# Optimization experiments

Hardware: AMD Instinct MI355X
Metric: run time of the kernel (lower is better)

The kernel has to match this reference:

```python
import jax, jax.numpy as jnp
import numpy as np

EPS = 1e-5

def ste_sign(x):
    # forward: sign(x) in {-1,+1}; backward: straight-through with |x|<=1 clip
    xc = jnp.clip(x, -1.0, 1.0)
    s = jnp.where(x >= 0, 1.0, -1.0).astype(x.dtype)
    return xc + jax.lax.stop_gradient(s - xc)

def quant_w(w):
    # 1-bit weight: sign(w) scaled by mean |w| (XNOR-Net style)
    return ste_sign(w) * jnp.mean(jnp.abs(w))

def qconv(x, w, stride, pad):
    # quantized conv: binarize activations and weights, then dense conv
    xq = ste_sign(x)
    wq = quant_w(w)
    return jax.lax.conv_general_dilated(
        xq, wq, window_strides=(stride, stride),
        padding=[(pad, pad), (pad, pad)],
        dimension_numbers=('NCHW', 'OIHW', 'NCHW'))

def batchnorm(x, gamma, beta):
    # training-mode BN: batch statistics over (N, H, W)
    mu = jnp.mean(x, axis=(0, 2, 3), keepdims=True)
    var = jnp.var(x, axis=(0, 2, 3), keepdims=True)
    xhat = (x - mu) * jax.lax.rsqrt(var + EPS)
    return xhat * gamma[None, :, None, None] + beta[None, :, None, None]

def setup_inputs() -> dict:
    key = jax.random.key(0)
    ks = jax.random.split(key, 4)
    in_planes, planes = 128, 256
    x = jax.random.normal(ks[0], (64, in_planes, 56, 56), dtype=jnp.float32)
    w1 = jax.random.normal(ks[1], (planes, in_planes, 3, 3), dtype=jnp.float32) * 0.05
    w2 = jax.random.normal(ks[2], (planes, planes, 3, 3), dtype=jnp.float32) * 0.05
    ws = jax.random.normal(ks[3], (planes, in_planes, 1, 1), dtype=jnp.float32) * 0.05
    g1 = jnp.ones((planes,), jnp.float32); b1 = jnp.zeros((planes,), jnp.float32)
    g2 = jnp.ones((planes,), jnp.float32); b2 = jnp.zeros((planes,), jnp.float32)
    return {'x': x, 'w1': w1, 'g1': g1, 'b1': b1, 'w2': w2, 'g2': g2, 'b2': b2, 'ws': ws}

def reference(x, w1, g1, b1, w2, g2, b2, ws):
    out = batchnorm(qconv(x, w1, stride=2, pad=1), g1, b1)   # [N,256,28,28]
    out = qconv(out, w2, stride=1, pad=1)
    out = out + qconv(x, ws, stride=2, pad=0)                # quantized 1x1 shortcut
    out = batchnorm(out, g2, b2)
    return out
```

## Files before the change

kernel.cpp:

```cpp
#include <hip/hip_runtime.h>
#include <stdint.h>

#define N_    64
#define CIN   128
#define CMID  256
#define H_    56
#define W_    56
#define OH    28
#define OW    28
#define NPIX  (OH*OW)
#define MPAD  800
#define MTOT  (N_*MPAD)
#define CNT_CH (N_*NPIX)
#define PXH   58
#define PYH   30
#define EPS_  1e-5f

#define STATS_BYTES 16384
#define OFF_PXI 16384
#define OFF_PYI (OFF_PXI + 27551744)
#define OFF_W1F (OFF_PYI + 14745600)
#define OFF_W2F (OFF_W1F + 294912)
#define OFF_WSF (OFF_W2F + 589824)
#define MEMSET_BYTES OFF_W1F

typedef int v4i  __attribute__((ext_vector_type(4)));
typedef int v16i __attribute__((ext_vector_type(16)));

#define MFMA_I8 __builtin_amdgcn_mfma_i32_32x32x32_i8

typedef const __attribute__((address_space(1))) void* gas_t;
typedef __attribute__((address_space(3))) void* las_t;

__device__ __forceinline__ void gl_lds16(const void* g, void* l) {
  __builtin_amdgcn_global_load_lds((gas_t)g, (las_t)l, 16, 0, 0);
}

__global__ __launch_bounds__(256) void reduce_abs_k(const float* __restrict__ w, int n,
                                                    float* __restrict__ out) {
  float s = 0.f;
  for (int i = blockIdx.x * 256 + threadIdx.x; i < n; i += gridDim.x * 256)
    s += fabsf(w[i]);
  for (int off = 32; off; off >>= 1) s += __shfl_down(s, off);
  if ((threadIdx.x & 63) == 0) atomicAdd(out, s);
}

__global__ __launch_bounds__(256) void pack_x_k(const float* __restrict__ x,
                                                int8_t* __restrict__ px) {
  int idx = blockIdx.x * 256 + threadIdx.x;
  int n = idx / (H_ * W_), hw = idx - n * (H_ * W_);
  int ih = hw / W_, iw = hw - ih * W_;
  const float* xp = x + ((size_t)n * CIN) * (H_ * W_) + hw;
  uint32_t wd[32];
#pragma unroll
  for (int c4 = 0; c4 < 32; ++c4) {
    uint32_t wv = 0u;
#pragma unroll
    for (int j = 0; j < 4; ++j) {
      uint32_t b = (xp[(size_t)(c4 * 4 + j) * (H_ * W_)] >= 0.f) ? 0x01u : 0xFFu;
      wv |= b << (j * 8);
    }
    wd[c4] = wv;
  }
  uint4* dst = (uint4*)(px + (((size_t)n * (PXH * PXH) + (ih + 1) * PXH + (iw + 1)) * CIN));
#pragma unroll
  for (int q = 0; q < 8; ++q)
    dst[q] = make_uint4(wd[q * 4], wd[q * 4 + 1], wd[q * 4 + 2], wd[q * 4 + 3]);
}

__global__ __launch_bounds__(256) void packw1f_k(const float* __restrict__ w1,
                                                 uint32_t* __restrict__ w1f) {
  int T = blockIdx.x * 256 + threadIdx.x;
  int l = T & 63, fb = T >> 6;
  int nb = fb & 7, kc = fb >> 3;
  int o = nb * 32 + (l & 31);
  int kbase = kc * 32 + (l >> 5) * 16;
  uint32_t wd[4] = {0u, 0u, 0u, 0u};
#pragma unroll
  for (int j = 0; j < 16; ++j) {
    int k = kbase + j, t = k >> 7, c = k & 127;
    uint32_t b = (w1[((size_t)o * CIN + c) * 9 + t] >= 0.f) ? 0x01u : 0xFFu;
    wd[j >> 2] |= b << ((j & 3) * 8);
  }
  ((uint4*)w1f)[T] = make_uint4(wd[0], wd[1], wd[2], wd[3]);
}

__global__ __launch_bounds__(256) void packw2f_k(const float* __restrict__ w2,
                                                 uint32_t* __restrict__ w2f) {
  int T = blockIdx.x * 256 + threadIdx.x;
  int l = T & 63, fb = T >> 6;
  int nb = fb & 7, kc = fb >> 3;
  int o = nb * 32 + (l & 31);
  int kbase = kc * 32 + (l >> 5) * 16;
  uint32_t wd[4] = {0u, 0u, 0u, 0u};
#pragma unroll
  for (int j = 0; j < 16; ++j) {
    int k = kbase + j, t = k >> 8, c = k & 255;
    uint32_t b = (w2[((size_t)o * CMID + c) * 9 + t] >= 0.f) ? 0x01u : 0xFFu;
    wd[j >> 2] |= b << ((j & 3) * 8);
  }
  ((uint4*)w2f)[T] = make_uint4(wd[0], wd[1], wd[2], wd[3]);
}

__global__ __launch_bounds__(256) void packwsf_k(const float* __restrict__ ws,
                                                 uint32_t* __restrict__ wsf) {
  int T = blockIdx.x * 256 + threadIdx.x;
  int l = T & 63, fb = T >> 6;
  int nb = fb & 7, kc = fb >> 3;
  int o = nb * 32 + (l & 31);
  int kbase = kc * 32 + (l >> 5) * 16;
  uint32_t wd[4] = {0u, 0u, 0u, 0u};
#pragma unroll
  for (int j = 0; j < 16; ++j) {
    int c = kbase + j;
    uint32_t b = (ws[(size_t)o * CIN + c] >= 0.f) ? 0x01u : 0xFFu;
    wd[j >> 2] |= b << ((j & 3) * 8);
  }
  ((uint4*)wsf)[T] = make_uint4(wd[0], wd[1], wd[2], wd[3]);
}

__global__ __launch_bounds__(256, 2) void conv1_k(const int8_t* __restrict__ px,
                                                  const uint8_t* __restrict__ w1f,
                                                  short* __restrict__ y16,
                                                  float* __restrict__ stats) {
  __shared__ int8_t lds[2][32768];
  int bnh = blockIdx.x & 1, bm = blockIdx.x >> 1;
  int tid = threadIdx.x, w = tid >> 6, l = tid & 63;
  int l31 = l & 31, lhi = l >> 5;
  int blockM = bm * 128;
  int waveM = blockM + (w & 1) * 64;
  int waveN = bnh * 128 + (w >> 1) * 64;
  int nbgl2 = (w >> 1) * 2;

  int srcsw = (((l & 7) ^ (l >> 3)) << 4);
  uint32_t rowoff[4];
#pragma unroll
  for (int i = 0; i < 4; ++i) {
    int p = blockM + (w * 4 + i) * 8 + (l >> 3);
    int n = p / MPAD, hw = p - n * MPAD;
    if (hw >= NPIX) hw = 0;
    int oh = hw / OW, ow = hw - oh * OW;
    rowoff[i] = (uint32_t)((n * (PXH * PXH) + (2 * oh) * PXH + 2 * ow) * CIN);
  }
  int sw = (l31 & 7) << 4;
  uint32_t aoff[2][4];
#pragma unroll
  for (int m = 0; m < 2; ++m) {
    int pxl = (w & 1) * 64 + m * 32 + l31;
#pragma unroll
    for (int kcl = 0; kcl < 4; ++kcl)
      aoff[m][kcl] = (uint32_t)(pxl * 128 + ((kcl * 32 + lhi * 16) ^ sw));
  }

  v16i acc[2][2] = {};

  auto stage = [&](int t, int8_t* buf) {
    int kh = t / 3, kw = t - 3 * kh;
    uint32_t tapoff = (uint32_t)((kh * PXH + kw) * CIN);
#pragma unroll
    for (int i = 0; i < 4; ++i) {
      int ch = w * 4 + i;
      gl_lds16(px + (size_t)(rowoff[i] + tapoff) + srcsw, buf + ch * 1024);
      gl_lds16(w1f + ((size_t)(((t * 4 + w) * 8) + bnh * 4 + i) << 10) + l * 16,
               buf + 16384 + ch * 1024);
    }
  };

  stage(0, lds[0]);
  __syncthreads();
  for (int it = 0; it < 9; ++it) {
    if (it < 8) stage(it + 1, lds[(it + 1) & 1]);
    const int8_t* cbuf = lds[it & 1];
    v4i a[2][4], b[2][4];
#pragma unroll
    for (int m = 0; m < 2; ++m)
#pragma unroll
      for (int kcl = 0; kcl < 4; ++kcl)
        a[m][kcl] = *(const v4i*)(cbuf + aoff[m][kcl]);
#pragma unroll
    for (int n2 = 0; n2 < 2; ++n2)
#pragma unroll
      for (int kcl = 0; kcl < 4; ++kcl)
        b[n2][kcl] = *(const v4i*)(cbuf + 16384 + (kcl * 4 + nbgl2 + n2) * 1024 + l * 16);
#pragma unroll
    for (int kcl = 0; kcl < 4; ++kcl) {
      acc[0][0] = MFMA_I8(a[0][kcl], b[0][kcl], acc[0][0], 0, 0, 0);
      acc[0][1] = MFMA_I8(a[0][kcl], b[1][kcl], acc[0][1], 0, 0, 0);
      acc[1][0] = MFMA_I8(a[1][kcl], b[0][kcl], acc[1][0], 0, 0, 0);
      acc[1][1] = MFMA_I8(a[1][kcl], b[1][kcl], acc[1][1], 0, 0, 0);
    }
    __syncthreads();
  }

#pragma unroll
  for (int n2 = 0; n2 < 2; ++n2) {
    int o = waveN + n2 * 32 + l31;
    float ssum = 0.f, ssq = 0.f;
#pragma unroll
    for (int m = 0; m < 2; ++m) {
      int tbase = waveM + m * 32;
      int nb0 = tbase / MPAD, r0 = tbase - nb0 * MPAD;
#pragma unroll
      for (int r = 0; r < 16; ++r) {
        int row = (r & 3) + 8 * (r >> 2) + 4 * lhi;
        int hwr = r0 + row;
        int d = acc[m][n2][r];
        bool valid = hwr < NPIX;
        if (valid) y16[((size_t)nb0 * NPIX + hwr) * CMID + o] = (short)d;
        float fd = valid ? (float)d : 0.f;
        ssum += fd; ssq += fd * fd;
      }
    }
    ssum += __shfl_down(ssum, 32);
    ssq  += __shfl_down(ssq, 32);
    if (l < 32) { atomicAdd(&stats[16 + o], ssum); atomicAdd(&stats[272 + o], ssq); }
  }
}

__global__ void bn1_prep_k(float* __restrict__ stats,
                           const float* __restrict__ g1,
                           const float* __restrict__ b1) {
  int c = threadIdx.x;
  float alpha1 = stats[0] * (1.f / (CMID * CIN * 9));
  float S = stats[16 + c], S2 = stats[272 + c];
  float mu = alpha1 * (S * (1.f / CNT_CH));
  float ey2 = alpha1 * alpha1 * (S2 * (1.f / CNT_CH));
  float var = fmaxf(ey2 - mu * mu, 0.f);
  float rs = rsqrtf(var + EPS_);
  float g = g1[c];
  stats[1552 + c] = g * rs * alpha1;
  stats[1808 + c] = b1[c] - g * rs * mu;
}

__global__ __launch_bounds__(256) void pack_y_k(const short* __restrict__ y16,
                                                const float* __restrict__ stats,
                                                int8_t* __restrict__ py) {
  int gid = blockIdx.x * 256 + threadIdx.x;
  int cg = gid & 31, pix = gid >> 5;
  int n = pix / NPIX, hw = pix - n * NPIX;
  int oh = hw / OW, ow = hw - oh * OW;
  uint4 raw = *(const uint4*)(y16 + (size_t)pix * CMID + cg * 8);
  const float* A = stats + 1552 + cg * 8;
  const float* B = stats + 1808 + cg * 8;
  float4 A0 = *(const float4*)A, A1 = *(const float4*)(A + 4);
  float4 B0 = *(const float4*)B, B1 = *(const float4*)(B + 4);
  int s[8];
  s[0] = (int)(short)(raw.x & 0xFFFF); s[1] = ((int)raw.x) >> 16;
  s[2] = (int)(short)(raw.y & 0xFFFF); s[3] = ((int)raw.y) >> 16;
  s[4] = (int)(short)(raw.z & 0xFFFF); s[5] = ((int)raw.z) >> 16;
  s[6] = (int)(short)(raw.w & 0xFFFF); s[7] = ((int)raw.w) >> 16;
  float a[8] = {A0.x, A0.y, A0.z, A0.w, A1.x, A1.y, A1.z, A1.w};
  float b[8] = {B0.x, B0.y, B0.z, B0.w, B1.x, B1.y, B1.z, B1.w};
  uint32_t w0 = 0u, w1 = 0u;
#pragma unroll
  for (int j = 0; j < 4; ++j) {
    w0 |= ((fmaf(a[j], (float)s[j], b[j]) >= 0.f) ? 0x01u : 0xFFu) << (j * 8);
    w1 |= ((fmaf(a[4 + j], (float)s[4 + j], b[4 + j]) >= 0.f) ? 0x01u : 0xFFu) << (j * 8);
  }
  size_t off = ((size_t)n * (PYH * PYH) + (oh + 1) * PYH + (ow + 1)) * CMID + cg * 8;
  *(uint2*)(py + off) = make_uint2(w0, w1);
}

__global__ __launch_bounds__(256, 2) void conv2_k(const int8_t* __restrict__ py,
                                                  const int8_t* __restrict__ px,
                                                  const uint8_t* __restrict__ w2f,
                                                  const uint8_t* __restrict__ wsf,
                                                  const float* __restrict__ stats,
                                                  float* __restrict__ out,
                                                  float* __restrict__ statw) {
  __shared__ int8_t lds[2][32768];
  int bnh = blockIdx.x & 1, bm = blockIdx.x >> 1;
  int tid = threadIdx.x, w = tid >> 6, l = tid & 63;
  int l31 = l & 31, lhi = l >> 5;
  int blockM = bm * 128;
  int waveM = blockM + (w & 1) * 64;
  int waveN = bnh * 128 + (w >> 1) * 64;
  int nbgl2 = (w >> 1) * 2;

  int srcsw = (((l & 7) ^ (l >> 3)) << 4);
  uint32_t rowoff[4], sxoff[4];
#pragma unroll
  for (int i = 0; i < 4; ++i) {
    int p = blockM + (w * 4 + i) * 8 + (l >> 3);
    int n = p / MPAD, hw = p - n * MPAD;
    if (hw >= NPIX) hw = 0;
    int oh = hw / OW, ow = hw - oh * OW;
    rowoff[i] = (uint32_t)((n * (PYH * PYH) + oh * PYH + ow) * CMID);
    sxoff[i]  = (uint32_t)((n * (PXH * PXH) + (2 * oh + 1) * PXH + (2 * ow + 1)) * CIN);
  }
  int sw = (l31 & 7) << 4;
  uint32_t aoff[2][4];
#pragma unroll
  for (int m = 0; m < 2; ++m) {
    int pxl = (w & 1) * 64 + m * 32 + l31;
#pragma unroll
    for (int kcl = 0; kcl < 4; ++kcl)
      aoff[m][kcl] = (uint32_t)(pxl * 128 + ((kcl * 32 + lhi * 16) ^ sw));
  }

  v16i am[2][2] = {};

  auto stageM = [&](int j, int8_t* buf) {
    int t = j >> 1, h = j & 1;
    int kh = t / 3, kw = t - 3 * kh;
    uint32_t tapoff = (uint32_t)((kh * PYH + kw) * CMID + h * 128);
    int kc = t * 8 + h * 4 + w;
#pragma unroll
    for (int i = 0; i < 4; ++i) {
      int ch = w * 4 + i;
      gl_lds16(py + (size_t)(rowoff[i] + tapoff) + srcsw, buf + ch * 1024);
      gl_lds16(w2f + ((size_t)(kc * 8 + bnh * 4 + i) << 10) + l * 16,
               buf + 16384 + ch * 1024);
    }
  };
  auto computeM = [&](const int8_t* cbuf, v16i (&acc)[2][2]) {
    v4i a[2][4], b[2][4];
#pragma unroll
    for (int m = 0; m < 2; ++m)
#pragma unroll
      for (int kcl = 0; kcl < 4; ++kcl)
        a[m][kcl] = *(const v4i*)(cbuf + aoff[m][kcl]);
#pragma unroll
    for (int n2 = 0; n2 < 2; ++n2)
#pragma unroll
      for (int kcl = 0; kcl < 4; ++kcl)
        b[n2][kcl] = *(const v4i*)(cbuf + 16384 + (kcl * 4 + nbgl2 + n2) * 1024 + l * 16);
#pragma unroll
    for (int kcl = 0; kcl < 4; ++kcl) {
      acc[0][0] = MFMA_I8(a[0][kcl], b[0][kcl], acc[0][0], 0, 0, 0);
      acc[0][1] = MFMA_I8(a[0][kcl], b[1][kcl], acc[0][1], 0, 0, 0);
      acc[1][0] = MFMA_I8(a[1][kcl], b[0][kcl], acc[1][0], 0, 0, 0);
      acc[1][1] = MFMA_I8(a[1][kcl], b[1][kcl], acc[1][1], 0, 0, 0);
    }
  };

  stageM(0, lds[0]);
  __syncthreads();
  for (int it = 0; it < 17; ++it) {
    stageM(it + 1, lds[(it + 1) & 1]);
    computeM(lds[it & 1], am);
    __syncthreads();
  }
  {
    int8_t* buf = lds[0];
#pragma unroll
    for (int i = 0; i < 4; ++i) {
      int ch = w * 4 + i;
      gl_lds16(px + (size_t)sxoff[i] + srcsw, buf + ch * 1024);
      gl_lds16(wsf + ((size_t)(w * 8 + bnh * 4 + i) << 10) + l * 16,
               buf + 16384 + ch * 1024);
    }
  }
  computeM(lds[1], am);
  __syncthreads();
  v16i as[2][2] = {};
  computeM(lds[0], as);

  float a2  = stats[1] * (1.f / (CMID * CMID * 9));
  float asx = stats[2] * (1.f / (CMID * CIN));
#pragma unroll
  for (int n2 = 0; n2 < 2; ++n2) {
    int o = waveN + n2 * 32 + l31;
    float ssum = 0.f, ssq = 0.f;
#pragma unroll
    for (int m = 0; m < 2; ++m) {
      int tbase = waveM + m * 32;
      int nb0 = tbase / MPAD, r0 = tbase - nb0 * MPAD;
#pragma unroll
      for (int r = 0; r < 16; ++r) {
        int row = (r & 3) + 8 * (r >> 2) + 4 * lhi;
        int hwr = r0 + row;
        bool valid = hwr < NPIX;
        float v = a2 * (float)am[m][n2][r] + asx * (float)as[m][n2][r];
        if (valid) out[((size_t)nb0 * CMID + o) * NPIX + hwr] = v;
        float vm = valid ? v : 0.f;
        ssum += vm; ssq += vm * vm;
      }
    }
    ssum += __shfl_down(ssum, 32);
    ssq  += __shfl_down(ssq, 32);
    if (l < 32) { atomicAdd(&statw[528 + o], ssum); atomicAdd(&statw[784 + o], ssq); }
  }
}

__global__ void bn2_prep_k(float* __restrict__ stats,
                           const float* __restrict__ g2,
                           const float* __restrict__ b2) {
  int c = threadIdx.x;
  float S = stats[528 + c], S2 = stats[784 + c];
  float mu = S * (1.f / CNT_CH);
  float var = fmaxf(S2 * (1.f / CNT_CH) - mu * mu, 0.f);
  float rs = rsqrtf(var + EPS_);
  float g = g2[c];
  stats[1040 + c] = g * rs;
  stats[1296 + c] = b2[c] - g * rs * mu;
}

__global__ __launch_bounds__(256) void bn2_apply_k(float4* __restrict__ out,
                                                   const float* __restrict__ stats) {
  int idx = blockIdx.x * 256 + threadIdx.x;
  int c = (idx / (NPIX / 4)) & (CMID - 1);
  float sc = stats[1040 + c], of = stats[1296 + c];
  float4 v = out[idx];
  v.x = v.x * sc + of; v.y = v.y * sc + of; v.z = v.z * sc + of; v.w = v.w * sc + of;
  out[idx] = v;
}

extern "C" void kernel_launch(void* const* d_in, const int* in_sizes, int n_in,
                              void* d_out, int out_size, void* d_ws, size_t ws_size,
                              hipStream_t stream) {
  const float* x   = (const float*)d_in[0];
  const float* w1  = (const float*)d_in[1];
  const float* g1  = (const float*)d_in[2];
  const float* b1  = (const float*)d_in[3];
  const float* w2  = (const float*)d_in[4];
  const float* g2  = (const float*)d_in[5];
  const float* b2  = (const float*)d_in[6];
  const float* wsc = (const float*)d_in[7];
  float* out = (float*)d_out;

  char* ws = (char*)d_ws;
  float*    stats = (float*)ws;
  int8_t*   pxi = (int8_t*)(ws + OFF_PXI);
  int8_t*   pyi = (int8_t*)(ws + OFF_PYI);
  uint32_t* w1f = (uint32_t*)(ws + OFF_W1F);
  uint32_t* w2f = (uint32_t*)(ws + OFF_W2F);
  uint32_t* wsf = (uint32_t*)(ws + OFF_WSF);
  short*    y16 = (short*)d_out;

  hipMemsetAsync(ws, 0, MEMSET_BYTES, stream);

  reduce_abs_k<<<128, 256, 0, stream>>>(w1,  CMID * CIN * 9,  &stats[0]);
  reduce_abs_k<<<256, 256, 0, stream>>>(w2,  CMID * CMID * 9, &stats[1]);
  reduce_abs_k<<<32,  256, 0, stream>>>(wsc, CMID * CIN,      &stats[2]);

  pack_x_k<<<784, 256, 0, stream>>>(x, pxi);
  packw1f_k<<<72, 256, 0, stream>>>(w1, w1f);
  packw2f_k<<<144, 256, 0, stream>>>(w2, w2f);
  packwsf_k<<<8, 256, 0, stream>>>(wsc, wsf);

  conv1_k<<<800, 256, 0, stream>>>(pxi, (const uint8_t*)w1f, y16, stats);
  bn1_prep_k<<<1, 256, 0, stream>>>(stats, g1, b1);
  pack_y_k<<<6272, 256, 0, stream>>>(y16, stats, pyi);
  conv2_k<<<800, 256, 0, stream>>>(pyi, pxi, (const uint8_t*)w2f, (const uint8_t*)wsf,
                                   stats, out, stats);
  bn2_prep_k<<<1, 256, 0, stream>>>(stats, g2, b2);
  bn2_apply_k<<<12544, 256, 0, stream>>>((float4*)out, stats);
}
```

Baseline: 372.2 us.

## Widen conv blocks to full N, add triple-buffered LDS pipeline with vmcnt waits

Both conv kernels now use 512-thread blocks that cover all 256 output channels, so the A tile is shared across the full N width and the grid halves to 400 blocks. Block order is remapped so that consecutive blocks are spread across M. Staging moves from double to triple buffering, using explicit s_waitcnt vmcnt(6) plus a raw barrier so two stages stay in flight. MFMA sections are wrapped in setprio. LDS grows to 144KB per block, which limits occupancy to one block per CU and could reduce latency hiding, despite the launch_bounds hint of 2.

```diff
diff --git a/kernel.cpp b/kernel.cpp
--- a/kernel.cpp
+++ b/kernel.cpp
@@ -36,6 +36,13 @@
   __builtin_amdgcn_global_load_lds((gas_t)g, (las_t)l, 16, 0, 0);
 }
 
+#define WAITVM6() asm volatile("s_waitcnt vmcnt(6) lgkmcnt(0)" ::: "memory")
+#define WAITVM0() asm volatile("s_waitcnt vmcnt(0) lgkmcnt(0)" ::: "memory")
+#define BAR()     __builtin_amdgcn_s_barrier()
+
+#define BUFSZ 49152
+#define BOFF  16384
+
 __global__ __launch_bounds__(256) void reduce_abs_k(const float* __restrict__ w, int n,
                                                     float* __restrict__ out) {
   float s = 0.f;
@@ -119,24 +126,24 @@
   ((uint4*)wsf)[T] = make_uint4(wd[0], wd[1], wd[2], wd[3]);
 }
 
-__global__ __launch_bounds__(256, 2) void conv1_k(const int8_t* __restrict__ px,
+__global__ __launch_bounds__(512, 2) void conv1_k(const int8_t* __restrict__ px,
                                                   const uint8_t* __restrict__ w1f,
                                                   short* __restrict__ y16,
                                                   float* __restrict__ stats) {
-  __shared__ int8_t lds[2][32768];
-  int bnh = blockIdx.x & 1, bm = blockIdx.x >> 1;
+  __shared__ int8_t lds[3][BUFSZ];
+  int bm = (blockIdx.x & 7) * 50 + (blockIdx.x >> 3);
   int tid = threadIdx.x, w = tid >> 6, l = tid & 63;
   int l31 = l & 31, lhi = l >> 5;
   int blockM = bm * 128;
   int waveM = blockM + (w & 1) * 64;
-  int waveN = bnh * 128 + (w >> 1) * 64;
-  int nbgl2 = (w >> 1) * 2;
+  int waveN = (w >> 1) * 64;
+  int nbg0 = (w >> 1) * 2;
 
   int srcsw = (((l & 7) ^ (l >> 3)) << 4);
-  uint32_t rowoff[4];
-#pragma unroll
-  for (int i = 0; i < 4; ++i) {
-    int p = blockM + (w * 4 + i) * 8 + (l >> 3);
+  uint32_t rowoff[2];
+#pragma unroll
+  for (int i = 0; i < 2; ++i) {
+    int p = blockM + (w * 2 + i) * 8 + (l >> 3);
     int n = p / MPAD, hw = p - n * MPAD;
     if (hw >= NPIX) hw = 0;
     int oh = hw / OW, ow = hw - oh * OW;
@@ -158,19 +165,16 @@
     int kh = t / 3, kw = t - 3 * kh;
     uint32_t tapoff = (uint32_t)((kh * PXH + kw) * CIN);
 #pragma unroll
-    for (int i = 0; i < 4; ++i) {
-      int ch = w * 4 + i;
-      gl_lds16(px + (size_t)(rowoff[i] + tapoff) + srcsw, buf + ch * 1024);
-      gl_lds16(w1f + ((size_t)(((t * 4 + w) * 8) + bnh * 4 + i) << 10) + l * 16,
-               buf + 16384 + ch * 1024);
+    for (int i = 0; i < 2; ++i)
+      gl_lds16(px + (size_t)(rowoff[i] + tapoff) + srcsw, buf + (w * 2 + i) * 1024);
+#pragma unroll
+    for (int i2 = 0; i2 < 4; ++i2) {
+      int f = w * 4 + i2, kcl = f >> 3, nb = f & 7;
+      gl_lds16(w1f + ((size_t)(((t * 4 + kcl) * 8) + nb) << 10) + l * 16,
+               buf + BOFF + f * 1024);
     }
   };
-
-  stage(0, lds[0]);
-  __syncthreads();
-  for (int it = 0; it < 9; ++it) {
-    if (it < 8) stage(it + 1, lds[(it + 1) & 1]);
-    const int8_t* cbuf = lds[it & 1];
+  auto compute = [&](const int8_t* cbuf, v16i (&ac)[2][2]) {
     v4i a[2][4], b[2][4];
 #pragma unroll
     for (int m = 0; m < 2; ++m)
@@ -181,16 +185,32 @@
     for (int n2 = 0; n2 < 2; ++n2)
 #pragma unroll
       for (int kcl = 0; kcl < 4; ++kcl)
-        b[n2][kcl] = *(const v4i*)(cbuf + 16384 + (kcl * 4 + nbgl2 + n2) * 1024 + l * 16);
+        b[n2][kcl] = *(const v4i*)(cbuf + BOFF + (kcl * 8 + nbg0 + n2) * 1024 + l * 16);
+    __builtin_amdgcn_s_setprio(1);
 #pragma unroll
     for (int kcl = 0; kcl < 4; ++kcl) {
-      acc[0][0] = MFMA_I8(a[0][kcl], b[0][kcl], acc[0][0], 0, 0, 0);
-      acc[0][1] = MFMA_I8(a[0][kcl], b[1][kcl], acc[0][1], 0, 0, 0);
-      acc[1][0] = MFMA_I8(a[1][kcl], b[0][kcl], acc[1][0], 0, 0, 0);
-      acc[1][1] = MFMA_I8(a[1][kcl], b[1][kcl], acc[1][1], 0, 0, 0);
-    }
-    __syncthreads();
-  }
+      ac[0][0] = MFMA_I8(a[0][kcl], b[0][kcl], ac[0][0], 0, 0, 0);
+      ac[0][1] = MFMA_I8(a[0][kcl], b[1][kcl], ac[0][1], 0, 0, 0);
+      ac[1][0] = MFMA_I8(a[1][kcl], b[0][kcl], ac[1][0], 0, 0, 0);
+      ac[1][1] = MFMA_I8(a[1][kcl], b[1][kcl], ac[1][1], 0, 0, 0);
+    }
+    __builtin_amdgcn_s_setprio(0);
+  };
+
+  int8_t* cur = &lds[0][0];
+  int8_t* nx1 = &lds[1][0];
+  int8_t* nx2 = &lds[2][0];
+  stage(0, cur); stage(1, nx1);
+  WAITVM6(); BAR();
+  for (int t = 0; t < 7; ++t) {
+    stage(t + 2, nx2);
+    compute(cur, acc);
+    WAITVM6(); BAR();
+    int8_t* tmp = cur; cur = nx1; nx1 = nx2; nx2 = tmp;
+  }
+  compute(cur, acc);
+  WAITVM0(); BAR();
+  compute(nx1, acc);
 
 #pragma unroll
   for (int n2 = 0; n2 < 2; ++n2) {
@@ -261,27 +281,27 @@
   *(uint2*)(py + off) = make_uint2(w0, w1);
 }
 
-__global__ __launch_bounds__(256, 2) void conv2_k(const int8_t* __restrict__ py,
+__global__ __launch_bounds__(512, 2) void conv2_k(const int8_t* __restrict__ py,
                                                   const int8_t* __restrict__ px,
                                                   const uint8_t* __restrict__ w2f,
                                                   const uint8_t* __restrict__ wsf,
                                                   const float* __restrict__ stats,
                                                   float* __restrict__ out,
                                                   float* __restrict__ statw) {
-  __shared__ int8_t lds[2][32768];
-  int bnh = blockIdx.x & 1, bm = blockIdx.x >> 1;
+  __shared__ int8_t lds[3][BUFSZ];
+  int bm = (blockIdx.x & 7) * 50 + (blockIdx.x >> 3);
   int tid = threadIdx.x, w = tid >> 6, l = tid & 63;
   int l31 = l & 31, lhi = l >> 5;
   int blockM = bm * 128;
   int waveM = blockM + (w & 1) * 64;
-  int waveN = bnh * 128 + (w >> 1) * 64;
-  int nbgl2 = (w >> 1) * 2;
+  int waveN = (w >> 1) * 64;
+  int nbg0 = (w >> 1) * 2;
 
   int srcsw = (((l & 7) ^ (l >> 3)) << 4);
-  uint32_t rowoff[4], sxoff[4];
-#pragma unroll
-  for (int i = 0; i < 4; ++i) {
-    int p = blockM + (w * 4 + i) * 8 + (l >> 3);
+  uint32_t rowoff[2], sxoff[2];
+#pragma unroll
+  for (int i = 0; i < 2; ++i) {
+    int p = blockM + (w * 2 + i) * 8 + (l >> 3);
     int n = p / MPAD, hw = p - n * MPAD;
     if (hw >= NPIX) hw = 0;
     int oh = hw / OW, ow = hw - oh * OW;
@@ -300,20 +320,32 @@
 
   v16i am[2][2] = {};
 
-  auto stageM = [&](int j, int8_t* buf) {
-    int t = j >> 1, h = j & 1;
-    int kh = t / 3, kw = t - 3 * kh;
-    uint32_t tapoff = (uint32_t)((kh * PYH + kw) * CMID + h * 128);
-    int kc = t * 8 + h * 4 + w;
-#pragma unroll
-    for (int i = 0; i < 4; ++i) {
-      int ch = w * 4 + i;
-      gl_lds16(py + (size_t)(rowoff[i] + tapoff) + srcsw, buf + ch * 1024);
-      gl_lds16(w2f + ((size_t)(kc * 8 + bnh * 4 + i) << 10) + l * 16,
-               buf + 16384 + ch * 1024);
+  auto stage = [&](int j, int8_t* buf) {
+    if (j < 18) {
+      int t = j >> 1, h = j & 1;
+      int kh = t / 3, kw = t - 3 * kh;
+      uint32_t tapoff = (uint32_t)((kh * PYH + kw) * CMID + h * 128);
+#pragma unroll
+      for (int i = 0; i < 2; ++i)
+        gl_lds16(py + (size_t)(rowoff[i] + tapoff) + srcsw, buf + (w * 2 + i) * 1024);
+#pragma unroll
+      for (int i2 = 0; i2 < 4; ++i2) {
+        int f = w * 4 + i2, kcl = f >> 3, nb = f & 7;
+        int kc = t * 8 + h * 4 + kcl;
+        gl_lds16(w2f + ((size_t)(kc * 8 + nb) << 10) + l * 16, buf + BOFF + f * 1024);
+      }
+    } else {
+#pragma unroll
+      for (int i = 0; i < 2; ++i)
+        gl_lds16(px + (size_t)sxoff[i] + srcsw, buf + (w * 2 + i) * 1024);
+#pragma unroll
+      for (int i2 = 0; i2 < 4; ++i2) {
+        int f = w * 4 + i2, kcl = f >> 3, nb = f & 7;
+        gl_lds16(wsf + ((size_t)(kcl * 8 + nb) << 10) + l * 16, buf + BOFF + f * 1024);
+      }
     }
   };
-  auto computeM = [&](const int8_t* cbuf, v16i (&acc)[2][2]) {
+  auto compute = [&](const int8_t* cbuf, v16i (&ac)[2][2]) {
     v4i a[2][4], b[2][4];
 #pragma unroll
     for (int m = 0; m < 2; ++m)
@@ -324,37 +356,33 @@
     for (int n2 = 0; n2 < 2; ++n2)
 #pragma unroll
       for (int kcl = 0; kcl < 4; ++kcl)
-        b[n2][kcl] = *(const v4i*)(cbuf + 16384 + (kcl * 4 + nbgl2 + n2) * 1024 + l * 16);
+        b[n2][kcl] = *(const v4i*)(cbuf + BOFF + (kcl * 8 + nbg0 + n2) * 1024 + l * 16);
+    __builtin_amdgcn_s_setprio(1);
 #pragma unroll
     for (int kcl = 0; kcl < 4; ++kcl) {
-      acc[0][0] = MFMA_I8(a[0][kcl], b[0][kcl], acc[0][0], 0, 0, 0);
-      acc[0][1] = MFMA_I8(a[0][kcl], b[1][kcl], acc[0][1], 0, 0, 0);
-      acc[1][0] = MFMA_I8(a[1][kcl], b[0][kcl], acc[1][0], 0, 0, 0);
-      acc[1][1] = MFMA_I8(a[1][kcl], b[1][kcl], acc[1][1], 0, 0, 0);
-    }
+      ac[0][0] = MFMA_I8(a[0][kcl], b[0][kcl], ac[0][0], 0, 0, 0);
+      ac[0][1] = MFMA_I8(a[0][kcl], b[1][kcl], ac[0][1], 0, 0, 0);
+      ac[1][0] = MFMA_I8(a[1][kcl], b[0][kcl], ac[1][0], 0, 0, 0);
+      ac[1][1] = MFMA_I8(a[1][kcl], b[1][kcl], ac[1][1], 0, 0, 0);
+    }
+    __builtin_amdgcn_s_setprio(0);
   };
 
-  stageM(0, lds[0]);
-  __syncthreads();
-  for (int it = 0; it < 17; ++it) {
-    stageM(it + 1, lds[(it + 1) & 1]);
-    computeM(lds[it & 1], am);
-    __syncthreads();
-  }
-  {
-    int8_t* buf = lds[0];
-#pragma unroll
-    for (int i = 0; i < 4; ++i) {
-      int ch = w * 4 + i;
-      gl_lds16(px + (size_t)sxoff[i] + srcsw, buf + ch * 1024);
-      gl_lds16(wsf + ((size_t)(w * 8 + bnh * 4 + i) << 10) + l * 16,
-               buf + 16384 + ch * 1024);
-    }
-  }
-  computeM(lds[1], am);
-  __syncthreads();
+  int8_t* cur = &lds[0][0];
+  int8_t* nx1 = &lds[1][0];
+  int8_t* nx2 = &lds[2][0];
+  stage(0, cur); stage(1, nx1);
+  WAITVM6(); BAR();
+  for (int t = 0; t < 17; ++t) {
+    stage(t + 2, nx2);
+    compute(cur, am);
+    WAITVM6(); BAR();
+    int8_t* tmp = cur; cur = nx1; nx1 = nx2; nx2 = tmp;
+  }
+  compute(cur, am);
+  WAITVM0(); BAR();
   v16i as[2][2] = {};
-  computeM(lds[0], as);
+  compute(nx1, as);
 
   float a2  = stats[1] * (1.f / (CMID * CMID * 9));
   float asx = stats[2] * (1.f / (CMID * CIN));
@@ -439,10 +467,10 @@
   packw2f_k<<<144, 256, 0, stream>>>(w2, w2f);
   packwsf_k<<<8, 256, 0, stream>>>(wsc, wsf);
 
-  conv1_k<<<800, 256, 0, stream>>>(pxi, (const uint8_t*)w1f, y16, stats);
+  conv1_k<<<400, 512, 0, stream>>>(pxi, (const uint8_t*)w1f, y16, stats);
   bn1_prep_k<<<1, 256, 0, stream>>>(stats, g1, b1);
   pack_y_k<<<6272, 256, 0, stream>>>(y16, stats, pyi);
-  conv2_k<<<800, 256, 0, stream>>>(pyi, pxi, (const uint8_t*)w2f, (const uint8_t*)wsf,
+  conv2_k<<<400, 512, 0, stream>>>(pyi, pxi, (const uint8_t*)w2f, (const uint8_t*)wsf,
                                    stats, out, stats);
   bn2_prep_k<<<1, 256, 0, stream>>>(stats, g2, b2);
   bn2_apply_k<<<12544, 256, 0, stream>>>((float4*)out, stats);
```

Result: no change. 379.4 us (+1.9%).
